# Kernel tuning notes

Hardware: AMD Instinct MI355X
Metric: run time of the kernel (lower is better)

The kernel has to match this reference:

```python
import jax, jax.numpy as jnp
import numpy as np

DIM = 512
MAX_STEP = 4
SLOTS = 8


def _lin(x, w, b):
    # torch nn.Linear convention: w is [out, in]
    return jnp.matmul(x, jnp.swapaxes(w, -1, -2)) + b


def setup_inputs() -> dict:
    B, L, HW, d, S, K = 512, 32, 196, DIM, MAX_STEP, SLOTS
    ks = iter(jax.random.split(jax.random.key(0), 48))
    def rn(shape, scale=1.0):
        return scale * jax.random.normal(next(ks), shape, dtype=jnp.float32)
    p = 0.05  # weight init scale
    z = lambda *s: jnp.zeros(s, jnp.float32)
    return {
        'context': rn((B, L, d)),
        'question': rn((B, 2 * d)),
        'knowledge': rn((B, d, HW)),
        'kb_proj': rn((B, d, HW)),
        'control': rn((B, d)),
        'memory': rn((B, d)),
        'history': rn((B, d, K)),
        'Wt_sequential': jnp.zeros((B, 1, K), jnp.float32).at[:, :, 0].set(1.0),
        # ControlUnit params (per-step position-aware linears, control-question linear, attention linear)
        'ctrl_pos_w': rn((S, d, 2 * d), p), 'ctrl_pos_b': z(S, d),
        'ctrl_cq_w': rn((d, 2 * d), p), 'ctrl_cq_b': z(d),
        'ctrl_attn_w': rn((1, d), p), 'ctrl_attn_b': z(1),
        # ReadUnit params (memory proj, concat proj, attention)
        'read_mem_w': rn((d, d), p), 'read_mem_b': z(d),
        'read_cat_w': rn((d, 2 * d), p), 'read_cat_b': z(d),
        'read_attn_w': rn((1, d), p), 'read_attn_b': z(1),
        # ReadMemory params (same structure, over the slot history)
        'rm_mem_w': rn((d, d), p), 'rm_mem_b': z(d),
        'rm_cat_w': rn((d, 2 * d), p), 'rm_cat_b': z(d),
        'rm_attn_w': rn((1, d), p), 'rm_attn_b': z(1),
        # WriteUnit (no self-attention / no memory gate)
        'write_w': rn((d, 2 * d), p), 'write_b': z(d),
        # linear_read gate MLP (2d -> 2d -> 1)
        'lr_w1': rn((2 * d, 2 * d), p), 'lr_b1': z(2 * d),
        'lr_w2': rn((1, 2 * d), p), 'lr_b2': z(1),
        # linear_read_history gate MLP
        'lrh_w1': rn((2 * d, 2 * d), p), 'lrh_b1': z(2 * d),
        'lrh_w2': rn((1, 2 * d), p), 'lrh_b2': z(1),
        # linear_layer_mix_context MLP (d -> d -> 3)
        'mix_w1': rn((d, d), p), 'mix_b1': z(d),
        'mix_w2': rn((3, d), p), 'mix_b2': z(3),
    }


def _forward(context, question, knowledge, kb_proj, control, memory, history, Wt_sequential,
             ctrl_pos_w, ctrl_pos_b, ctrl_cq_w, ctrl_cq_b, ctrl_attn_w, ctrl_attn_b,
             read_mem_w, read_mem_b, read_cat_w, read_cat_b, read_attn_w, read_attn_b,
             rm_mem_w, rm_mem_b, rm_cat_w, rm_cat_b, rm_attn_w, rm_attn_b,
             write_w, write_b, lr_w1, lr_b1, lr_w2, lr_b2,
             lrh_w1, lrh_b1, lrh_w2, lrh_b2, mix_w1, mix_b1, mix_w2, mix_b2):
    K = history.shape[2]
    # shift-by-one circulant matrix, matches the hard-coded convolution_kernel for slots in {4,6,8}
    conv_kernel = jnp.roll(jnp.eye(K, dtype=history.dtype), -1, axis=1)
    for i in range(MAX_STEP):
        # --- ControlUnit: attention over contextual words ---
        pa = _lin(question, ctrl_pos_w[i], ctrl_pos_b[i])                                  # [B,d]
        cqi = _lin(jnp.concatenate([control, pa], axis=1), ctrl_cq_w, ctrl_cq_b)           # [B,d]
        cvi = jax.nn.softmax(_lin(cqi[:, None, :] * context, ctrl_attn_w, ctrl_attn_b), axis=1)  # [B,L,1]
        control = jnp.sum(cvi * context, axis=1)                                           # [B,d]
        # --- ReadUnit: attention over the knowledge base ---
        mem_p = _lin(memory, read_mem_w, read_mem_b)[:, :, None]                           # [B,d,1]
        cat = jnp.concatenate([mem_p * kb_proj, kb_proj], axis=1)                          # [B,2d,HW]
        feat = _lin(cat.transpose(0, 2, 1), read_cat_w, read_cat_b)                        # [B,HW,d]
        attn = jax.nn.softmax(_lin(feat * control[:, None, :], read_attn_w, read_attn_b), axis=1)
        attn = attn.transpose(0, 2, 1)                                                     # [B,1,HW]
        read = jnp.sum(attn * knowledge, axis=2)                                           # [B,d]
        # --- ReadMemory: attention over the slot history ---
        memh = _lin(memory, rm_mem_w, rm_mem_b)[:, :, None]                                # [B,d,1]
        cath = jnp.concatenate([memh * history, history], axis=1)                          # [B,2d,K]
        feath = _lin(cath.transpose(0, 2, 1), rm_cat_w, rm_cat_b)                          # [B,K,d]
        rvi_h = jax.nn.softmax(_lin(feath * control[:, None, :], rm_attn_w, rm_attn_b), axis=1).transpose(0, 2, 1)  # [B,1,K]
        read_h = jnp.sum(rvi_h * history, axis=2)                                          # [B,d]
        # --- gates ---
        gkb = jax.nn.sigmoid(_lin(jax.nn.elu(_lin(jnp.concatenate([control, read], axis=1), lr_w1, lr_b1)), lr_w2, lr_b2))      # [B,1]
        gmem = jax.nn.sigmoid(_lin(jax.nn.elu(_lin(jnp.concatenate([control, read_h], axis=1), lrh_w1, lrh_b1)), lrh_w2, lrh_b2))  # [B,1]
        # --- gated addressable memory write (NTM-style) ---
        wts = Wt_sequential[:, 0, :]                                                       # [B,K]
        W = (gmem * rvi_h[:, 0, :] + wts * (1.0 - gmem)) * gkb                             # [B,K]
        history = history * (1.0 - W[:, None, :]) + read[:, :, None] * W[:, None, :]       # erase + add
        first = (1.0 - gmem) * gkb                                                         # [B,1]
        Wt_sequential = ((wts @ conv_kernel) * first + wts * (1.0 - first))[:, None, :]    # [B,1,K]
        # --- context mixing + write ---
        now_ctx = gkb * read
        last_ctx = gmem * read_h
        latest_ctx = (1.0 - gkb) * last_ctx + now_ctx
        cwv = jax.nn.softmax(_lin(jax.nn.elu(_lin(control, mix_w1, mix_b1)), mix_w2, mix_b2), axis=1)  # [B,3]
        ctx_read = cwv[:, 0:1] * now_ctx + cwv[:, 1:2] * last_ctx + cwv[:, 2:3] * latest_ctx
        memory = _lin(jnp.concatenate([ctx_read, memory], axis=1), write_w, write_b)       # [B,d]
    return memory


reference = _forward
```

## Files before the change

kernel.cpp:

```cpp
#include <hip/hip_runtime.h>
#include <cstddef>

constexpr int NB   = 512;
constexpr int ND   = 512;
constexpr int NL   = 32;
constexpr int NHW  = 196;
constexpr int NK   = 8;
constexpr int NSTEP = 4;

typedef __attribute__((ext_vector_type(8))) short short8v;
typedef __attribute__((ext_vector_type(4))) short short4v;
typedef __attribute__((ext_vector_type(4))) float f32x4;

__device__ __forceinline__ void splitbf(float x, short& h, short& l) {
    unsigned u  = __float_as_uint(x);
    unsigned hb = (u + 0x7FFFu + ((u >> 16) & 1u)) & 0xFFFF0000u;
    h = (short)(hb >> 16);
    float rem = x - __uint_as_float(hb);
    unsigned v = __float_as_uint(rem);
    l = (short)((v + 0x7FFFu + ((v >> 16) & 1u)) >> 16);
}

struct GP {
    const float* A1; const float* A2;
    const short* Bh; const short* Bl;
    const float* bias; float* C;
    int lda1, lda2, k1, N, K, ntN, tile0;
};
struct GP3 { GP p[3]; int np; };

template<int ACT>
__global__ __launch_bounds__(256) void ggemm_k(GP3 g)
{
    __shared__ short Ah[32][32], Al[32][32], Bh_s[64][32], Bl_s[64][32];
    const int flat = blockIdx.x;
    int pi = 0;
    if (g.np > 1 && flat >= g.p[1].tile0) pi = 1;
    if (g.np > 2 && flat >= g.p[2].tile0) pi = 2;
    const GP p = g.p[pi];
    const int local = flat - p.tile0;
    const int my = local / p.ntN;
    const int nx = local - my * p.ntN;
    const int m0 = my * 32, n0 = nx * 64;
    const int t = threadIdx.x, lane = t & 63, wid = t >> 6;
    const int wr = wid >> 1, wc = wid & 1;
    const int lr = lane & 15, lk = (lane >> 4) * 8;
    const int asr = t >> 3, asc = (t & 7) * 4;
    const int bsr = t >> 2, bsk = (t & 3) * 8;
    f32x4 acc0 = {}, acc1 = {};

    for (int kt = 0; kt < p.K; kt += 32) {
        {
            const int gk = kt + asc;
            const float* src = (gk < p.k1) ? p.A1 + (size_t)(m0 + asr) * p.lda1 + gk
                                           : p.A2 + (size_t)(m0 + asr) * p.lda2 + (gk - p.k1);
            float4 x = *(const float4*)src;
            short4v vh, vl; short hh, ll;
            splitbf(x.x, hh, ll); vh[0] = hh; vl[0] = ll;
            splitbf(x.y, hh, ll); vh[1] = hh; vl[1] = ll;
            splitbf(x.z, hh, ll); vh[2] = hh; vl[2] = ll;
            splitbf(x.w, hh, ll); vh[3] = hh; vl[3] = ll;
            *(short4v*)&Ah[asr][asc] = vh;
            *(short4v*)&Al[asr][asc] = vl;
        }
        {
            const size_t boff = (size_t)(n0 + bsr) * p.K + kt + bsk;
            *(short8v*)&Bh_s[bsr][bsk] = *(const short8v*)(p.Bh + boff);
            *(short8v*)&Bl_s[bsr][bsk] = *(const short8v*)(p.Bl + boff);
        }
        __syncthreads();
        short8v ah  = *(short8v*)&Ah[wr * 16 + lr][lk];
        short8v al  = *(short8v*)&Al[wr * 16 + lr][lk];
        short8v bh0 = *(short8v*)&Bh_s[wc * 32      + lr][lk];
        short8v bh1 = *(short8v*)&Bh_s[wc * 32 + 16 + lr][lk];
        short8v bl0 = *(short8v*)&Bl_s[wc * 32      + lr][lk];
        short8v bl1 = *(short8v*)&Bl_s[wc * 32 + 16 + lr][lk];
        acc0 = __builtin_amdgcn_mfma_f32_16x16x32_bf16(ah, bh0, acc0, 0, 0, 0);
        acc1 = __builtin_amdgcn_mfma_f32_16x16x32_bf16(ah, bh1, acc1, 0, 0, 0);
        acc0 = __builtin_amdgcn_mfma_f32_16x16x32_bf16(al, bh0, acc0, 0, 0, 0);
        acc1 = __builtin_amdgcn_mfma_f32_16x16x32_bf16(al, bh1, acc1, 0, 0, 0);
        acc0 = __builtin_amdgcn_mfma_f32_16x16x32_bf16(ah, bl0, acc0, 0, 0, 0);
        acc1 = __builtin_amdgcn_mfma_f32_16x16x32_bf16(ah, bl1, acc1, 0, 0, 0);
        __syncthreads();
    }
    const int r0 = m0 + wr * 16 + (lane >> 4) * 4;
    const int cb = n0 + wc * 32 + lr;
    #pragma unroll
    for (int fc = 0; fc < 2; ++fc) {
        const f32x4& a = fc ? acc1 : acc0;
        const int col = cb + fc * 16;
        float badd = p.bias ? p.bias[col] : 0.f;
        #pragma unroll
        for (int rr = 0; rr < 4; ++rr) {
            float x = a[rr] + badd;
            if (ACT == 1) x = (x > 0.f) ? x : (expf(x) - 1.f);
            p.C[(size_t)(r0 + rr) * p.N + col] = x;
        }
    }
}

struct WSeg { const float* src; short* dh; short* dl; int n; };
struct WTab { WSeg s[8]; int total; };

__global__ __launch_bounds__(256) void wconv_k(WTab tab)
{
    int i = blockIdx.x * 256 + threadIdx.x;
    if (i >= tab.total) return;
    int seg = 0, off = i;
    while (off >= tab.s[seg].n) { off -= tab.s[seg].n; ++seg; }
    short h, l; splitbf(tab.s[seg].src[off], h, l);
    tab.s[seg].dh[off] = h;
    tab.s[seg].dl[off] = l;
}

__global__ __launch_bounds__(256) void tconv_k(
    const float* s0, short* dh0, short* dl0,
    const float* s1, short* dh1, short* dl1)
{
    const float* src = blockIdx.z ? s1 : s0;
    short* dh = blockIdx.z ? dh1 : dh0;
    short* dl = blockIdx.z ? dl1 : dl0;
    __shared__ float tile[32][33];
    const int n0 = blockIdx.x * 32, k0 = blockIdx.y * 32;
    const int tx = threadIdx.x & 31, ty = threadIdx.x >> 5;
    for (int i = ty; i < 32; i += 8)
        tile[i][tx] = src[(size_t)(k0 + i) * 1024 + n0 + tx];
    __syncthreads();
    for (int i = ty; i < 32; i += 8) {
        short h, l; splitbf(tile[tx][i], h, l);
        dh[(size_t)(n0 + i) * 512 + k0 + tx] = h;
        dl[(size_t)(n0 + i) * 512 + k0 + tx] = l;
    }
}

__global__ __launch_bounds__(512) void ctrl_attn_k(
    const float* __restrict__ cqi, const float* __restrict__ context,
    const float* __restrict__ attn_w, const float* __restrict__ read_attn_w,
    const float* __restrict__ rm_attn_w,
    float* __restrict__ control, float* __restrict__ cw, float* __restrict__ cwh)
{
    const int b = blockIdx.x, t = threadIdx.x;
    const int lane = t & 63, w = t >> 6;
    __shared__ float q[ND];
    __shared__ float p[NL];
    const float* ctx = context + (size_t)b * NL * ND;

    q[t] = cqi[(size_t)b * ND + t] * attn_w[t];
    __syncthreads();

    for (int l = w; l < NL; l += 8) {
        float s = 0.f;
        const float* row = ctx + (size_t)l * ND;
        #pragma unroll
        for (int d = lane; d < ND; d += 64) s += q[d] * row[d];
        #pragma unroll
        for (int o = 32; o; o >>= 1) s += __shfl_down(s, o);
        if (lane == 0) p[l] = s;
    }
    __syncthreads();
    if (t == 0) {
        float mx = p[0];
        for (int l = 1; l < NL; ++l) mx = fmaxf(mx, p[l]);
        float sum = 0.f;
        for (int l = 0; l < NL; ++l) { float e = expf(p[l] - mx); p[l] = e; sum += e; }
        const float inv = 1.f / sum;
        for (int l = 0; l < NL; ++l) p[l] *= inv;
    }
    __syncthreads();
    float a = 0.f;
    #pragma unroll 8
    for (int l = 0; l < NL; ++l) a += p[l] * ctx[(size_t)l * ND + t];
    control[(size_t)b * ND + t] = a;
    cw [(size_t)b * ND + t] = a * read_attn_w[t];
    cwh[(size_t)b * ND + t] = a * rm_attn_w[t];
}

__global__ __launch_bounds__(256) void kbsh_k(
    const float* __restrict__ kb_proj, const float* __restrict__ mpc,
    const float* __restrict__ u, float* __restrict__ s_part,
    const float* __restrict__ hist, const float* __restrict__ uh,
    float* __restrict__ rvi, float* __restrict__ read_h)
{
    __shared__ float sh[NK * ND + ND];
    __shared__ float sred[NK], pk[NK];
    const int bx = blockIdx.x, t = threadIdx.x;
    const int lane = t & 63, w = t >> 6;

    if (bx < 4 * NB) {
        const int jc = bx >> 9, b = bx & 511;
        float* v = sh;
        const int j0 = jc * 128;
        if (t < 128) {
            const int j = j0 + t;
            v[t] = mpc[(size_t)b * 1024 + j] * u[(size_t)b * 1024 + j]
                 + u[(size_t)b * 1024 + 512 + j];
        }
        __syncthreads();
        if (t < NHW) {
            const float* base = kb_proj + (size_t)b * ND * NHW + (size_t)j0 * NHW + t;
            float s = 0.f;
            #pragma unroll 8
            for (int j = 0; j < 128; ++j) s += base[(size_t)j * NHW] * v[j];
            s_part[((size_t)jc * NB + b) * 200 + t] = s;
        }
    } else {
        const int b = bx - 4 * NB;
        float* ht = sh;
        float* vh = sh + NK * ND;
        const float* hb = hist + (size_t)b * ND * NK;

        for (int dd = t; dd < ND; dd += 256) {
            float4 h0 = *(const float4*)&hb[(size_t)dd * NK];
            float4 h1 = *(const float4*)&hb[(size_t)dd * NK + 4];
            ht[0 * ND + dd] = h0.x; ht[1 * ND + dd] = h0.y;
            ht[2 * ND + dd] = h0.z; ht[3 * ND + dd] = h0.w;
            ht[4 * ND + dd] = h1.x; ht[5 * ND + dd] = h1.y;
            ht[6 * ND + dd] = h1.z; ht[7 * ND + dd] = h1.w;
            vh[dd] = mpc[(size_t)b * 1024 + 512 + dd] * uh[(size_t)b * 1024 + dd]
                   + uh[(size_t)b * 1024 + 512 + dd];
        }
        __syncthreads();

        for (int k = w; k < NK; k += 4) {
            float s = 0.f;
            #pragma unroll 4
            for (int dd = lane; dd < ND; dd += 64) s += ht[k * ND + dd] * vh[dd];
            #pragma unroll
            for (int o = 32; o; o >>= 1) s += __shfl_down(s, o);
            if (lane == 0) sred[k] = s;
        }
        __syncthreads();
        if (t == 0) {
            float mx = sred[0];
            #pragma unroll
            for (int k = 1; k < NK; ++k) mx = fmaxf(mx, sred[k]);
            float ev[NK]; float sum = 0.f;
            #pragma unroll
            for (int k = 0; k < NK; ++k) { ev[k] = expf(sred[k] - mx); sum += ev[k]; }
            const float inv = 1.f / sum;
            #pragma unroll
            for (int k = 0; k < NK; ++k) { float pv = ev[k] * inv; pk[k] = pv; rvi[(size_t)b * NK + k] = pv; }
        }
        __syncthreads();
        for (int dd = t; dd < ND; dd += 256) {
            float a = 0.f;
            #pragma unroll
            for (int k = 0; k < NK; ++k) a += pk[k] * ht[k * ND + dd];
            read_h[(size_t)b * ND + dd] = a;
        }
    }
}

__global__ __launch_bounds__(256) void kb_read_k(
    const float* __restrict__ knowledge, const float* __restrict__ s_part,
    float* __restrict__ readv)
{
    const int dcb = blockIdx.x, b = blockIdx.y, t = threadIdx.x;
    const int lane = t & 63, w = t >> 6;
    __shared__ float ps[200];
    __shared__ float red[8];

    float val = -INFINITY;
    if (t < NHW) {
        float sp = 0.f;
        #pragma unroll
        for (int jc = 0; jc < 4; ++jc) sp += s_part[((size_t)jc * NB + b) * 200 + t];
        val = sp;
    }
    float mx = val;
    #pragma unroll
    for (int o = 32; o; o >>= 1) mx = fmaxf(mx, __shfl_xor(mx, o));
    if (lane == 0) red[w] = mx;
    __syncthreads();
    mx = fmaxf(fmaxf(red[0], red[1]), fmaxf(red[2], red[3]));
    const float e = (t < NHW) ? expf(val - mx) : 0.f;
    float sm = e;
    #pragma unroll
    for (int o = 32; o; o >>= 1) sm += __shfl_xor(sm, o);
    if (lane == 0) red[4 + w] = sm;
    __syncthreads();
    const float tot = red[4] + red[5] + red[6] + red[7];
    if (t < 200) ps[t] = (t < NHW) ? e / tot : 0.f;
    __syncthreads();

    const float* knw = knowledge + (size_t)b * ND * NHW;
    const int d1 = dcb * 64 + 64;
    for (int d = dcb * 64 + w; d < d1; d += 4) {
        const float* row = knw + (size_t)d * NHW;
        float a = 0.f;
        for (int h = lane; h < NHW; h += 64) a += ps[h] * row[h];
        #pragma unroll
        for (int o = 32; o; o >>= 1) a += __shfl_down(a, o);
        if (lane == 0) readv[(size_t)b * ND + d] = a;
    }
}

__global__ __launch_bounds__(256) void update2_k(
    const float* __restrict__ g1a, const float* __restrict__ g1b,
    const float* __restrict__ m1,
    const float* __restrict__ lr_w2,  const float* __restrict__ lr_b2,
    const float* __restrict__ lrh_w2, const float* __restrict__ lrh_b2,
    const float* __restrict__ mix_w2, const float* __restrict__ mix_b2,
    const float* __restrict__ rvi, const float* __restrict__ readv,
    const float* __restrict__ read_h,
    float* __restrict__ hist, float* __restrict__ wts, float* __restrict__ ctx_read)
{
    const int b = blockIdx.x, t = threadIdx.x;
    const int lane = t & 63, w = t >> 6;
    __shared__ float red[4][5];
    __shared__ float sc[5];

    float pa = 0.f, pb = 0.f, p0 = 0.f, p1 = 0.f, p2 = 0.f;
    for (int k = t; k < 2 * ND; k += 256) {
        pa += g1a[(size_t)b * 2 * ND + k] * lr_w2[k];
        pb += g1b[(size_t)b * 2 * ND + k] * lrh_w2[k];
    }
    for (int d = t; d < ND; d += 256) {
        const float m = m1[(size_t)b * ND + d];
        p0 += m * mix_w2[d];
        p1 += m * mix_w2[ND + d];
        p2 += m * mix_w2[2 * ND + d];
    }
    #pragma unroll
    for (int o = 32; o; o >>= 1) {
        pa += __shfl_down(pa, o); pb += __shfl_down(pb, o);
        p0 += __shfl_down(p0, o); p1 += __shfl_down(p1, o); p2 += __shfl_down(p2, o);
    }
    if (lane == 0) { red[w][0] = pa; red[w][1] = pb; red[w][2] = p0; red[w][3] = p1; red[w][4] = p2; }
    __syncthreads();
    if (t == 0) {
        float sa = 0.f, sb = 0.f, s0 = 0.f, s1 = 0.f, s2 = 0.f;
        #pragma unroll
        for (int i = 0; i < 4; ++i) { sa += red[i][0]; sb += red[i][1]; s0 += red[i][2]; s1 += red[i][3]; s2 += red[i][4]; }
        sc[0] = 1.f / (1.f + expf(-(sa + lr_b2[0])));
        sc[1] = 1.f / (1.f + expf(-(sb + lrh_b2[0])));
        const float l0 = s0 + mix_b2[0], l1 = s1 + mix_b2[1], l2 = s2 + mix_b2[2];
        const float mx = fmaxf(l0, fmaxf(l1, l2));
        const float e0 = expf(l0 - mx), e1 = expf(l1 - mx), e2 = expf(l2 - mx);
        const float inv = 1.f / (e0 + e1 + e2);
        sc[2] = e0 * inv; sc[3] = e1 * inv; sc[4] = e2 * inv;
    }
    __syncthreads();

    const float gk = sc[0], gm = sc[1];
    const float c0 = sc[2], c1 = sc[3], c2 = sc[4];
    __shared__ float wo[NK], Ws[NK];
    if (t < NK) {
        const float w_old = wts[(size_t)b * NK + t];
        wo[t] = w_old;
        Ws[t] = (gm * rvi[(size_t)b * NK + t] + w_old * (1.f - gm)) * gk;
    }
    __syncthreads();
    float Wr[NK];
    #pragma unroll
    for (int k = 0; k < NK; ++k) Wr[k] = Ws[k];

    for (int dd = t; dd < ND; dd += 256) {
        const float rd = readv[(size_t)b * ND + dd];
        const float rh = read_h[(size_t)b * ND + dd];
        const float now = gk * rd, last = gm * rh;
        const float latest = (1.f - gk) * last + now;
        ctx_read[(size_t)b * ND + dd] = c0 * now + c1 * last + c2 * latest;
        float* hp = hist + (size_t)b * ND * NK + (size_t)dd * NK;
        float4 h0 = *(const float4*)&hp[0];
        float4 h1 = *(const float4*)&hp[4];
        h0.x = h0.x * (1.f - Wr[0]) + rd * Wr[0];
        h0.y = h0.y * (1.f - Wr[1]) + rd * Wr[1];
        h0.z = h0.z * (1.f - Wr[2]) + rd * Wr[2];
        h0.w = h0.w * (1.f - Wr[3]) + rd * Wr[3];
        h1.x = h1.x * (1.f - Wr[4]) + rd * Wr[4];
        h1.y = h1.y * (1.f - Wr[5]) + rd * Wr[5];
        h1.z = h1.z * (1.f - Wr[6]) + rd * Wr[6];
        h1.w = h1.w * (1.f - Wr[7]) + rd * Wr[7];
        *(float4*)&hp[0] = h0;
        *(float4*)&hp[4] = h1;
    }
    if (t == 0) {
        const float first = (1.f - gm) * gk;
        float nw[NK];
        #pragma unroll
        for (int k = 0; k < NK; ++k) nw[k] = wo[(k + 1) & 7] * first + wo[k] * (1.f - first);
        #pragma unroll
        for (int k = 0; k < NK; ++k) wts[(size_t)b * NK + k] = nw[k];
    }
}

extern "C" void kernel_launch(void* const* d_in, const int* in_sizes, int n_in,
                              void* d_out, int out_size, void* d_ws, size_t ws_size,
                              hipStream_t stream)
{
    (void)in_sizes; (void)n_in; (void)out_size; (void)ws_size;
    const float* context    = (const float*)d_in[0];
    const float* question   = (const float*)d_in[1];
    const float* knowledge  = (const float*)d_in[2];
    const float* kb_proj    = (const float*)d_in[3];
    const float* control0   = (const float*)d_in[4];
    const float* memory0    = (const float*)d_in[5];
    const float* history0   = (const float*)d_in[6];
    const float* wt0        = (const float*)d_in[7];
    const float* ctrl_pos_w = (const float*)d_in[8];
    const float* ctrl_pos_b = (const float*)d_in[9];
    const float* ctrl_cq_w  = (const float*)d_in[10];
    const float* ctrl_cq_b  = (const float*)d_in[11];
    const float* ctrl_attn_w= (const float*)d_in[12];
    const float* read_mem_w = (const float*)d_in[14];
    const float* read_mem_b = (const float*)d_in[15];
    const float* read_cat_w = (const float*)d_in[16];
    const float* read_attn_w= (const float*)d_in[18];
    const float* rm_mem_w   = (const float*)d_in[20];
    const float* rm_mem_b   = (const float*)d_in[21];
    const float* rm_cat_w   = (const float*)d_in[22];
    const float* rm_attn_w  = (const float*)d_in[24];
    const float* write_w    = (const float*)d_in[26];
    const float* write_b    = (const float*)d_in[27];
    const float* lr_w1      = (const float*)d_in[28];
    const float* lr_b1      = (const float*)d_in[29];
    const float* lr_w2      = (const float*)d_in[30];
    const float* lr_b2      = (const float*)d_in[31];
    const float* lrh_w1     = (const float*)d_in[32];
    const float* lrh_b1     = (const float*)d_in[33];
    const float* lrh_w2     = (const float*)d_in[34];
    const float* lrh_b2     = (const float*)d_in[35];
    const float* mix_w1     = (const float*)d_in[36];
    const float* mix_b1     = (const float*)d_in[37];
    const float* mix_w2     = (const float*)d_in[38];
    const float* mix_b2     = (const float*)d_in[39];

    float* f = (float*)d_ws;
    auto takef = [&](size_t n) { float* p = f; f += n; return p; };
    float* pa_all = takef((size_t)NB * 2048);
    float* cqi    = takef((size_t)NB * ND);
    float* control= takef((size_t)NB * ND);
    float* cw     = takef((size_t)NB * ND);
    float* cwh    = takef((size_t)NB * ND);
    float* mpc    = takef((size_t)NB * 1024);
    float* u      = takef((size_t)NB * 1024);
    float* uh     = takef((size_t)NB * 1024);
    float* readv  = takef((size_t)NB * ND);
    float* read_h = takef((size_t)NB * ND);
    float* rvi    = takef((size_t)NB * NK);
    float* g1a    = takef((size_t)NB * 1024);
    float* g1b    = takef((size_t)NB * 1024);
    float* m1buf  = takef((size_t)NB * ND);
    float* ctx    = takef((size_t)NB * ND);
    float* hist   = takef((size_t)NB * ND * NK);
    float* wts    = takef((size_t)NB * NK);
    float* memA   = takef((size_t)NB * ND);
    float* memB   = takef((size_t)NB * ND);
    float* s_part = takef((size_t)4 * NB * 200);
    float* bcat   = takef(1024);

    short* s = (short*)f;
    auto takes = [&](size_t n) { short* p = s; s += n; return p; };
    short* cpw_h = takes((size_t)2048 * 1024); short* cpw_l = takes((size_t)2048 * 1024);
    short* cqw_h = takes((size_t)512 * 1024);  short* cqw_l = takes((size_t)512 * 1024);
    short* wmc_h = takes((size_t)1024 * 512);  short* wmc_l = takes((size_t)1024 * 512);
    short* rcw_h = takes((size_t)1024 * 512);  short* rcw_l = takes((size_t)1024 * 512);
    short* rmw_h = takes((size_t)1024 * 512);  short* rmw_l = takes((size_t)1024 * 512);
    short* lrw_h = takes((size_t)1024 * 1024); short* lrw_l = takes((size_t)1024 * 1024);
    short* lhw_h = takes((size_t)1024 * 1024); short* lhw_l = takes((size_t)1024 * 1024);
    short* mxw_h = takes((size_t)512 * 512);   short* mxw_l = takes((size_t)512 * 512);
    short* ww_h  = takes((size_t)512 * 1024);  short* ww_l  = takes((size_t)512 * 1024);

    hipMemcpyAsync(hist, history0, sizeof(float) * NB * ND * NK, hipMemcpyDeviceToDevice, stream);
    hipMemcpyAsync(wts,  wt0,      sizeof(float) * NB * NK,      hipMemcpyDeviceToDevice, stream);
    hipMemcpyAsync(bcat,       read_mem_b, sizeof(float) * 512, hipMemcpyDeviceToDevice, stream);
    hipMemcpyAsync(bcat + 512, rm_mem_b,   sizeof(float) * 512, hipMemcpyDeviceToDevice, stream);

    WTab tab;
    tab.s[0] = {ctrl_pos_w, cpw_h, cpw_l, 2048 * 1024};
    tab.s[1] = {ctrl_cq_w,  cqw_h, cqw_l, 512 * 1024};
    tab.s[2] = {read_mem_w, wmc_h, wmc_l, 512 * 512};
    tab.s[3] = {rm_mem_w,   wmc_h + 512 * 512, wmc_l + 512 * 512, 512 * 512};
    tab.s[4] = {lr_w1,  lrw_h, lrw_l, 1024 * 1024};
    tab.s[5] = {lrh_w1, lhw_h, lhw_l, 1024 * 1024};
    tab.s[6] = {mix_w1, mxw_h, mxw_l, 512 * 512};
    tab.s[7] = {write_w, ww_h, ww_l, 512 * 1024};
    tab.total = 2048*1024 + 512*1024 + 512*512 + 512*512 + 1024*1024 + 1024*1024 + 512*512 + 512*1024;
    wconv_k<<<dim3((tab.total + 255) / 256), dim3(256), 0, stream>>>(tab);
    tconv_k<<<dim3(32, 16, 2), dim3(256), 0, stream>>>(read_cat_w, rcw_h, rcw_l,
                                                       rm_cat_w,  rmw_h, rmw_l);

    auto P = [](const float* A1, const float* A2, int lda1, int lda2, int k1,
                const short* Bh, const short* Bl, const float* bias, float* C,
                int N, int K, int tile0) {
        GP q; q.A1 = A1; q.A2 = A2; q.Bh = Bh; q.Bl = Bl; q.bias = bias; q.C = C;
        q.lda1 = lda1; q.lda2 = lda2; q.k1 = k1; q.N = N; q.K = K;
        q.ntN = N / 64; q.tile0 = tile0;
        return q;
    };
    auto tilesOf = [](int N) { return (N / 64) * (NB / 32); };
    auto GG = [&](GP3 g, int total, int act) {
        if (act) ggemm_k<1><<<dim3(total), dim3(256), 0, stream>>>(g);
        else     ggemm_k<0><<<dim3(total), dim3(256), 0, stream>>>(g);
    };

    {
        GP3 g; g.np = 1;
        g.p[0] = P(question, question, 1024, 1024, 1024, cpw_h, cpw_l, ctrl_pos_b, pa_all, 2048, 1024, 0);
        GG(g, tilesOf(2048), 0);
    }

    const float* mems[5] = {memory0, memA, memB, memA, (float*)d_out};
    const float* ctrl_cur = control0;

    for (int i = 0; i < NSTEP; ++i) {
        {
            GP3 g; int nt = 0, np = 0;
            if (i > 0) {
                g.p[np++] = P(ctx, mems[i - 1], ND, ND, ND, ww_h, ww_l, write_b,
                              (float*)mems[i], ND, 1024, nt);
                nt += tilesOf(ND);
            }
            g.p[np++] = P(ctrl_cur, pa_all + (size_t)i * ND, ND, 2048, ND,
                          cqw_h, cqw_l, ctrl_cq_b, cqi, ND, 1024, nt);
            nt += tilesOf(ND);
            g.np = np;
            GG(g, nt, 0);
        }
        ctrl_attn_k<<<dim3(NB), dim3(512), 0, stream>>>(cqi, context, ctrl_attn_w,
                                                        read_attn_w, rm_attn_w, control, cw, cwh);
        ctrl_cur = control;
        {
            GP3 g; g.np = 3;
            g.p[0] = P(mems[i], mems[i], ND, ND, ND, wmc_h, wmc_l, bcat, mpc, 1024, 512, 0);
            g.p[1] = P(cw,  cw,  ND, ND, ND, rcw_h, rcw_l, nullptr, u,  1024, 512, 256);
            g.p[2] = P(cwh, cwh, ND, ND, ND, rmw_h, rmw_l, nullptr, uh, 1024, 512, 512);
            GG(g, 768, 0);
        }
        kbsh_k<<<dim3(5 * NB), dim3(256), 0, stream>>>(kb_proj, mpc, u, s_part,
                                                       hist, uh, rvi, read_h);
        kb_read_k<<<dim3(8, NB), dim3(256), 0, stream>>>(knowledge, s_part, readv);
        {
            GP3 g; g.np = 3;
            g.p[0] = P(control, readv,  ND, ND, ND, lrw_h, lrw_l, lr_b1,  g1a, 1024, 1024, 0);
            g.p[1] = P(control, read_h, ND, ND, ND, lhw_h, lhw_l, lrh_b1, g1b, 1024, 1024, 256);
            g.p[2] = P(control, control, ND, ND, ND, mxw_h, mxw_l, mix_b1, m1buf, 512, 512, 512);
            GG(g, 640, 1);
        }
        update2_k<<<dim3(NB), dim3(256), 0, stream>>>(g1a, g1b, m1buf,
                                                      lr_w2, lr_b2, lrh_w2, lrh_b2,
                                                      mix_w2, mix_b2, rvi, readv, read_h,
                                                      hist, wts, ctx);
    }
    {
        GP3 g; g.np = 1;
        g.p[0] = P(ctx, mems[3], ND, ND, ND, ww_h, ww_l, write_b, (float*)mems[4], ND, 1024, 0);
        GG(g, tilesOf(ND), 0);
    }
}
```

Before: 960.7 us.

## Pre-split GEMM activations to bf16 hi/lo and cache bf16 knowledge tensors

Producer kernels now write activations straight into bf16 high/low pairs. The GEMM loads its MFMA operands directly from global memory without LDS staging, splitting or barriers. On the first step, kb_proj and knowledge are also converted to single bf16 and stored. Later steps read those bf16 copies, halving the traffic over the large knowledge tensors. This reduces precision for the knowledge reads and drops LDS reuse in the GEMM, and it needs a larger workspace.

After: 1.216 ms. 1.27x slower.

```diff
diff --git a/kernel.cpp b/kernel.cpp
--- a/kernel.cpp
+++ b/kernel.cpp
@@ -9,7 +9,6 @@
 constexpr int NSTEP = 4;
 
 typedef __attribute__((ext_vector_type(8))) short short8v;
-typedef __attribute__((ext_vector_type(4))) short short4v;
 typedef __attribute__((ext_vector_type(4))) float f32x4;
 
 __device__ __forceinline__ void splitbf(float x, short& h, short& l) {
@@ -20,87 +19,90 @@
     unsigned v = __float_as_uint(rem);
     l = (short)((v + 0x7FFFu + ((v >> 16) & 1u)) >> 16);
 }
+__device__ __forceinline__ unsigned short f2bf(float x) {
+    unsigned u = __float_as_uint(x);
+    return (unsigned short)((u + 0x7FFFu + ((u >> 16) & 1u)) >> 16);
+}
+__device__ __forceinline__ float bf2f(unsigned short h) {
+    return __uint_as_float(((unsigned)h) << 16);
+}
 
 struct GP {
-    const float* A1; const float* A2;
-    const short* Bh; const short* Bl;
-    const float* bias; float* C;
+    const short *A1h, *A1l, *A2h, *A2l;
+    const short *Bh, *Bl;
+    const float* bias;
+    float* C; short* Ch; short* Cl;
     int lda1, lda2, k1, N, K, ntN, tile0;
 };
-struct GP3 { GP p[3]; int np; };
+struct GPG { GP p[3]; int np; };
 
 template<int ACT>
-__global__ __launch_bounds__(256) void ggemm_k(GP3 g)
-{
-    __shared__ short Ah[32][32], Al[32][32], Bh_s[64][32], Bl_s[64][32];
+__global__ __launch_bounds__(256) void ggemm_k(GPG g)
+{
     const int flat = blockIdx.x;
     int pi = 0;
     if (g.np > 1 && flat >= g.p[1].tile0) pi = 1;
     if (g.np > 2 && flat >= g.p[2].tile0) pi = 2;
     const GP p = g.p[pi];
     const int local = flat - p.tile0;
-    const int my = local / p.ntN;
-    const int nx = local - my * p.ntN;
+    const int my = local / p.ntN, nx = local - my * p.ntN;
     const int m0 = my * 32, n0 = nx * 64;
-    const int t = threadIdx.x, lane = t & 63, wid = t >> 6;
+    const int lane = threadIdx.x & 63, wid = threadIdx.x >> 6;
     const int wr = wid >> 1, wc = wid & 1;
     const int lr = lane & 15, lk = (lane >> 4) * 8;
-    const int asr = t >> 3, asc = (t & 7) * 4;
-    const int bsr = t >> 2, bsk = (t & 3) * 8;
+
+    const int arow = m0 + wr * 16 + lr;
+    const int br0  = n0 + wc * 32 + lr;
+    const short* b0h = p.Bh + (size_t)br0 * p.K + lk;
+    const short* b0l = p.Bl + (size_t)br0 * p.K + lk;
+    const short* b1h = b0h + (size_t)16 * p.K;
+    const short* b1l = b0l + (size_t)16 * p.K;
+    const short* a1h = p.A1h + (size_t)arow * p.lda1 + lk;
+    const short* a1l = p.A1l + (size_t)arow * p.lda1 + lk;
+    const short* a2h = p.A2h + (size_t)arow * p.lda2 + lk;
+    const short* a2l = p.A2l + (size_t)arow * p.lda2 + lk;
+
     f32x4 acc0 = {}, acc1 = {};
-
     for (int kt = 0; kt < p.K; kt += 32) {
-        {
-            const int gk = kt + asc;
-            const float* src = (gk < p.k1) ? p.A1 + (size_t)(m0 + asr) * p.lda1 + gk
-                                           : p.A2 + (size_t)(m0 + asr) * p.lda2 + (gk - p.k1);
-            float4 x = *(const float4*)src;
-            short4v vh, vl; short hh, ll;
-            splitbf(x.x, hh, ll); vh[0] = hh; vl[0] = ll;
-            splitbf(x.y, hh, ll); vh[1] = hh; vl[1] = ll;
-            splitbf(x.z, hh, ll); vh[2] = hh; vl[2] = ll;
-            splitbf(x.w, hh, ll); vh[3] = hh; vl[3] = ll;
-            *(short4v*)&Ah[asr][asc] = vh;
-            *(short4v*)&Al[asr][asc] = vl;
-        }
-        {
-            const size_t boff = (size_t)(n0 + bsr) * p.K + kt + bsk;
-            *(short8v*)&Bh_s[bsr][bsk] = *(const short8v*)(p.Bh + boff);
-            *(short8v*)&Bl_s[bsr][bsk] = *(const short8v*)(p.Bl + boff);
-        }
-        __syncthreads();
-        short8v ah  = *(short8v*)&Ah[wr * 16 + lr][lk];
-        short8v al  = *(short8v*)&Al[wr * 16 + lr][lk];
-        short8v bh0 = *(short8v*)&Bh_s[wc * 32      + lr][lk];
-        short8v bh1 = *(short8v*)&Bh_s[wc * 32 + 16 + lr][lk];
-        short8v bl0 = *(short8v*)&Bl_s[wc * 32      + lr][lk];
-        short8v bl1 = *(short8v*)&Bl_s[wc * 32 + 16 + lr][lk];
-        acc0 = __builtin_amdgcn_mfma_f32_16x16x32_bf16(ah, bh0, acc0, 0, 0, 0);
-        acc1 = __builtin_amdgcn_mfma_f32_16x16x32_bf16(ah, bh1, acc1, 0, 0, 0);
-        acc0 = __builtin_amdgcn_mfma_f32_16x16x32_bf16(al, bh0, acc0, 0, 0, 0);
-        acc1 = __builtin_amdgcn_mfma_f32_16x16x32_bf16(al, bh1, acc1, 0, 0, 0);
-        acc0 = __builtin_amdgcn_mfma_f32_16x16x32_bf16(ah, bl0, acc0, 0, 0, 0);
-        acc1 = __builtin_amdgcn_mfma_f32_16x16x32_bf16(ah, bl1, acc1, 0, 0, 0);
-        __syncthreads();
-    }
-    const int r0 = m0 + wr * 16 + (lane >> 4) * 4;
+        short8v ah, al;
+        if (kt < p.k1) {
+            ah = *(const short8v*)(a1h + kt);
+            al = *(const short8v*)(a1l + kt);
+        } else {
+            ah = *(const short8v*)(a2h + (kt - p.k1));
+            al = *(const short8v*)(a2l + (kt - p.k1));
+        }
+        short8v v0h = *(const short8v*)(b0h + kt);
+        short8v v0l = *(const short8v*)(b0l + kt);
+        short8v v1h = *(const short8v*)(b1h + kt);
+        short8v v1l = *(const short8v*)(b1l + kt);
+        acc0 = __builtin_amdgcn_mfma_f32_16x16x32_bf16(ah, v0h, acc0, 0, 0, 0);
+        acc1 = __builtin_amdgcn_mfma_f32_16x16x32_bf16(ah, v1h, acc1, 0, 0, 0);
+        acc0 = __builtin_amdgcn_mfma_f32_16x16x32_bf16(al, v0h, acc0, 0, 0, 0);
+        acc1 = __builtin_amdgcn_mfma_f32_16x16x32_bf16(al, v1h, acc1, 0, 0, 0);
+        acc0 = __builtin_amdgcn_mfma_f32_16x16x32_bf16(ah, v0l, acc0, 0, 0, 0);
+        acc1 = __builtin_amdgcn_mfma_f32_16x16x32_bf16(ah, v1l, acc1, 0, 0, 0);
+    }
+    const int r0 = m0 + wr * 16 + ((lane >> 4) << 2);
     const int cb = n0 + wc * 32 + lr;
     #pragma unroll
     for (int fc = 0; fc < 2; ++fc) {
         const f32x4& a = fc ? acc1 : acc0;
         const int col = cb + fc * 16;
-        float badd = p.bias ? p.bias[col] : 0.f;
+        const float badd = p.bias ? p.bias[col] : 0.f;
         #pragma unroll
         for (int rr = 0; rr < 4; ++rr) {
             float x = a[rr] + badd;
             if (ACT == 1) x = (x > 0.f) ? x : (expf(x) - 1.f);
-            p.C[(size_t)(r0 + rr) * p.N + col] = x;
+            const size_t idx = (size_t)(r0 + rr) * p.N + col;
+            if (p.C) p.C[idx] = x;
+            if (p.Ch) { short h, l; splitbf(x, h, l); p.Ch[idx] = h; p.Cl[idx] = l; }
         }
     }
 }
 
 struct WSeg { const float* src; short* dh; short* dl; int n; };
-struct WTab { WSeg s[8]; int total; };
+struct WTab { WSeg s[12]; int total; };
 
 __global__ __launch_bounds__(256) void wconv_k(WTab tab)
 {
@@ -137,7 +139,9 @@
     const float* __restrict__ cqi, const float* __restrict__ context,
     const float* __restrict__ attn_w, const float* __restrict__ read_attn_w,
     const float* __restrict__ rm_attn_w,
-    float* __restrict__ control, float* __restrict__ cw, float* __restrict__ cwh)
+    short* __restrict__ ct_h, short* __restrict__ ct_l,
+    short* __restrict__ cw_h, short* __restrict__ cw_l,
+    short* __restrict__ cx_h, short* __restrict__ cx_l)
 {
     const int b = blockIdx.x, t = threadIdx.x;
     const int lane = t & 63, w = t >> 6;
@@ -170,16 +174,21 @@
     float a = 0.f;
     #pragma unroll 8
     for (int l = 0; l < NL; ++l) a += p[l] * ctx[(size_t)l * ND + t];
-    control[(size_t)b * ND + t] = a;
-    cw [(size_t)b * ND + t] = a * read_attn_w[t];
-    cwh[(size_t)b * ND + t] = a * rm_attn_w[t];
-}
-
+    const size_t ix = (size_t)b * ND + t;
+    short h, l2;
+    splitbf(a, h, l2);                     ct_h[ix] = h; ct_l[ix] = l2;
+    splitbf(a * read_attn_w[t], h, l2);    cw_h[ix] = h; cw_l[ix] = l2;
+    splitbf(a * rm_attn_w[t],  h, l2);     cx_h[ix] = h; cx_l[ix] = l2;
+}
+
+template<int FIRST>
 __global__ __launch_bounds__(256) void kbsh_k(
-    const float* __restrict__ kb_proj, const float* __restrict__ mpc,
-    const float* __restrict__ u, float* __restrict__ s_part,
+    const float* __restrict__ kbp_f32, unsigned short* __restrict__ kbp_bf,
+    const float* __restrict__ mpc, const float* __restrict__ u,
+    float* __restrict__ s_part,
     const float* __restrict__ hist, const float* __restrict__ uh,
-    float* __restrict__ rvi, float* __restrict__ read_h)
+    float* __restrict__ rvi, float* __restrict__ read_h,
+    short* __restrict__ rh_h, short* __restrict__ rh_l)
 {
     __shared__ float sh[NK * ND + ND];
     __shared__ float sred[NK], pk[NK];
@@ -197,10 +206,19 @@
         }
         __syncthreads();
         if (t < NHW) {
-            const float* base = kb_proj + (size_t)b * ND * NHW + (size_t)j0 * NHW + t;
+            const size_t base = (size_t)b * ND * NHW + (size_t)j0 * NHW + t;
             float s = 0.f;
-            #pragma unroll 8
-            for (int j = 0; j < 128; ++j) s += base[(size_t)j * NHW] * v[j];
+            #pragma unroll 4
+            for (int j = 0; j < 128; ++j) {
+                float x;
+                if (FIRST) {
+                    x = kbp_f32[base + (size_t)j * NHW];
+                    kbp_bf[base + (size_t)j * NHW] = f2bf(x);
+                } else {
+                    x = bf2f(kbp_bf[base + (size_t)j * NHW]);
+                }
+                s += x * v[j];
+            }
             s_part[((size_t)jc * NB + b) * 200 + t] = s;
         }
     } else {
@@ -246,14 +264,19 @@
             float a = 0.f;
             #pragma unroll
             for (int k = 0; k < NK; ++k) a += pk[k] * ht[k * ND + dd];
-            read_h[(size_t)b * ND + dd] = a;
-        }
-    }
-}
-
+            const size_t ix = (size_t)b * ND + dd;
+            read_h[ix] = a;
+            short h, l; splitbf(a, h, l);
+            rh_h[ix] = h; rh_l[ix] = l;
+        }
+    }
+}
+
+template<int FIRST>
 __global__ __launch_bounds__(256) void kb_read_k(
-    const float* __restrict__ knowledge, const float* __restrict__ s_part,
-    float* __restrict__ readv)
+    const float* __restrict__ knw_f32, unsigned short* __restrict__ knw_bf,
+    const float* __restrict__ s_part,
+    float* __restrict__ readv, short* __restrict__ rv_h, short* __restrict__ rv_l)
 {
     const int dcb = blockIdx.x, b = blockIdx.y, t = threadIdx.x;
     const int lane = t & 63, w = t >> 6;
@@ -283,15 +306,28 @@
     if (t < 200) ps[t] = (t < NHW) ? e / tot : 0.f;
     __syncthreads();
 
-    const float* knw = knowledge + (size_t)b * ND * NHW;
     const int d1 = dcb * 64 + 64;
     for (int d = dcb * 64 + w; d < d1; d += 4) {
-        const float* row = knw + (size_t)d * NHW;
+        const size_t rbase = (size_t)b * ND * NHW + (size_t)d * NHW;
         float a = 0.f;
-        for (int h = lane; h < NHW; h += 64) a += ps[h] * row[h];
+        for (int h = lane; h < NHW; h += 64) {
+            float x;
+            if (FIRST) {
+                x = knw_f32[rbase + h];
+                knw_bf[rbase + h] = f2bf(x);
+            } else {
+                x = bf2f(knw_bf[rbase + h]);
+            }
+            a += ps[h] * x;
+        }
         #pragma unroll
         for (int o = 32; o; o >>= 1) a += __shfl_down(a, o);
-        if (lane == 0) readv[(size_t)b * ND + d] = a;
+        if (lane == 0) {
+            const size_t ix = (size_t)b * ND + d;
+            readv[ix] = a;
+            short h2, l2; splitbf(a, h2, l2);
+            rv_h[ix] = h2; rv_l[ix] = l2;
+        }
     }
 }
 
@@ -303,7 +339,8 @@
     const float* __restrict__ mix_w2, const float* __restrict__ mix_b2,
     const float* __restrict__ rvi, const float* __restrict__ readv,
     const float* __restrict__ read_h,
-    float* __restrict__ hist, float* __restrict__ wts, float* __restrict__ ctx_read)
+    float* __restrict__ hist, float* __restrict__ wts,
+    short* __restrict__ ctx_h, short* __restrict__ ctx_l)
 {
     const int b = blockIdx.x, t = threadIdx.x;
     const int lane = t & 63, w = t >> 6;
@@ -360,7 +397,10 @@
         const float rh = read_h[(size_t)b * ND + dd];
         const float now = gk * rd, last = gm * rh;
         const float latest = (1.f - gk) * last + now;
-        ctx_read[(size_t)b * ND + dd] = c0 * now + c1 * last + c2 * latest;
+        const float cr = c0 * now + c1 * last + c2 * latest;
+        short h2, l2; splitbf(cr, h2, l2);
+        ctx_h[(size_t)b * ND + dd] = h2;
+        ctx_l[(size_t)b * ND + dd] = l2;
         float* hp = hist + (size_t)b * ND * NK + (size_t)dd * NK;
         float4 h0 = *(const float4*)&hp[0];
         float4 h1 = *(const float4*)&hp[4];
@@ -428,11 +468,7 @@
 
     float* f = (float*)d_ws;
     auto takef = [&](size_t n) { float* p = f; f += n; return p; };
-    float* pa_all = takef((size_t)NB * 2048);
     float* cqi    = takef((size_t)NB * ND);
-    float* control= takef((size_t)NB * ND);
-    float* cw     = takef((size_t)NB * ND);
-    float* cwh    = takef((size_t)NB * ND);
     float* mpc    = takef((size_t)NB * 1024);
     float* u      = takef((size_t)NB * 1024);
     float* uh     = takef((size_t)NB * 1024);
@@ -442,15 +478,13 @@
     float* g1a    = takef((size_t)NB * 1024);
     float* g1b    = takef((size_t)NB * 1024);
     float* m1buf  = takef((size_t)NB * ND);
-    float* ctx    = takef((size_t)NB * ND);
     float* hist   = takef((size_t)NB * ND * NK);
     float* wts    = takef((size_t)NB * NK);
-    float* memA   = takef((size_t)NB * ND);
-    float* memB   = takef((size_t)NB * ND);
     float* s_part = takef((size_t)4 * NB * 200);
     float* bcat   = takef(1024);
 
-    short* s = (short*)f;
+    uintptr_t fa = ((uintptr_t)f + 15) & ~(uintptr_t)15;
+    short* s = (short*)fa;
     auto takes = [&](size_t n) { short* p = s; s += n; return p; };
     short* cpw_h = takes((size_t)2048 * 1024); short* cpw_l = takes((size_t)2048 * 1024);
     short* cqw_h = takes((size_t)512 * 1024);  short* cqw_l = takes((size_t)512 * 1024);
@@ -461,6 +495,21 @@
     short* lhw_h = takes((size_t)1024 * 1024); short* lhw_l = takes((size_t)1024 * 1024);
     short* mxw_h = takes((size_t)512 * 512);   short* mxw_l = takes((size_t)512 * 512);
     short* ww_h  = takes((size_t)512 * 1024);  short* ww_l  = takes((size_t)512 * 1024);
+    short* q_h   = takes((size_t)512 * 1024);  short* q_l   = takes((size_t)512 * 1024);
+    short* c0_h  = takes((size_t)NB * ND);     short* c0_l  = takes((size_t)NB * ND);
+    short* m0_h  = takes((size_t)NB * ND);     short* m0_l  = takes((size_t)NB * ND);
+    short* pa_h  = takes((size_t)NB * 2048);   short* pa_l  = takes((size_t)NB * 2048);
+    short* ct_h  = takes((size_t)NB * ND);     short* ct_l  = takes((size_t)NB * ND);
+    short* cw_h  = takes((size_t)NB * ND);     short* cw_l  = takes((size_t)NB * ND);
+    short* cwh_h = takes((size_t)NB * ND);     short* cwh_l = takes((size_t)NB * ND);
+    short* rv_h  = takes((size_t)NB * ND);     short* rv_l  = takes((size_t)NB * ND);
+    short* rh_h  = takes((size_t)NB * ND);     short* rh_l  = takes((size_t)NB * ND);
+    short* cx_h  = takes((size_t)NB * ND);     short* cx_l  = takes((size_t)NB * ND);
+    short* mA_h  = takes((size_t)NB * ND);     short* mA_l  = takes((size_t)NB * ND);
+    short* mB_h  = takes((size_t)NB * ND);     short* mB_l  = takes((size_t)NB * ND);
+    short* mC_h  = takes((size_t)NB * ND);     short* mC_l  = takes((size_t)NB * ND);
+    unsigned short* kbp_bf = (unsigned short*)s;
+    unsigned short* knw_bf = kbp_bf + (size_t)NB * ND * NHW;
 
     hipMemcpyAsync(hist, history0, sizeof(float) * NB * ND * NK, hipMemcpyDeviceToDevice, stream);
     hipMemcpyAsync(wts,  wt0,      sizeof(float) * NB * NK,      hipMemcpyDeviceToDevice, stream);
@@ -468,84 +517,112 @@
     hipMemcpyAsync(bcat + 512, rm_mem_b,   sizeof(float) * 512, hipMemcpyDeviceToDevice, stream);
 
     WTab tab;
-    tab.s[0] = {ctrl_pos_w, cpw_h, cpw_l, 2048 * 1024};
-    tab.s[1] = {ctrl_cq_w,  cqw_h, cqw_l, 512 * 1024};
-    tab.s[2] = {read_mem_w, wmc_h, wmc_l, 512 * 512};
-    tab.s[3] = {rm_mem_w,   wmc_h + 512 * 512, wmc_l + 512 * 512, 512 * 512};
-    tab.s[4] = {lr_w1,  lrw_h, lrw_l, 1024 * 1024};
-    tab.s[5] = {lrh_w1, lhw_h, lhw_l, 1024 * 1024};
-    tab.s[6] = {mix_w1, mxw_h, mxw_l, 512 * 512};
-    tab.s[7] = {write_w, ww_h, ww_l, 512 * 1024};
-    tab.total = 2048*1024 + 512*1024 + 512*512 + 512*512 + 1024*1024 + 1024*1024 + 512*512 + 512*1024;
+    tab.s[0]  = {ctrl_pos_w, cpw_h, cpw_l, 2048 * 1024};
+    tab.s[1]  = {ctrl_cq_w,  cqw_h, cqw_l, 512 * 1024};
+    tab.s[2]  = {read_mem_w, wmc_h, wmc_l, 512 * 512};
+    tab.s[3]  = {rm_mem_w,   wmc_h + 512 * 512, wmc_l + 512 * 512, 512 * 512};
+    tab.s[4]  = {lr_w1,  lrw_h, lrw_l, 1024 * 1024};
+    tab.s[5]  = {lrh_w1, lhw_h, lhw_l, 1024 * 1024};
+    tab.s[6]  = {mix_w1, mxw_h, mxw_l, 512 * 512};
+    tab.s[7]  = {write_w, ww_h, ww_l, 512 * 1024};
+    tab.s[8]  = {question, q_h, q_l, 512 * 1024};
+    tab.s[9]  = {control0, c0_h, c0_l, 512 * 512};
+    tab.s[10] = {memory0,  m0_h, m0_l, 512 * 512};
+    tab.s[11] = {nullptr, nullptr, nullptr, 0};
+    tab.total = 2048*1024 + 512*1024 + 512*512 + 512*512 + 1024*1024 + 1024*1024
+              + 512*512 + 512*1024 + 512*1024 + 512*512 + 512*512;
     wconv_k<<<dim3((tab.total + 255) / 256), dim3(256), 0, stream>>>(tab);
     tconv_k<<<dim3(32, 16, 2), dim3(256), 0, stream>>>(read_cat_w, rcw_h, rcw_l,
                                                        rm_cat_w,  rmw_h, rmw_l);
 
-    auto P = [](const float* A1, const float* A2, int lda1, int lda2, int k1,
-                const short* Bh, const short* Bl, const float* bias, float* C,
-                int N, int K, int tile0) {
-        GP q; q.A1 = A1; q.A2 = A2; q.Bh = Bh; q.Bl = Bl; q.bias = bias; q.C = C;
+    auto P = [](const short* A1h, const short* A1l, int lda1, int k1,
+                const short* A2h, const short* A2l, int lda2,
+                const short* Bh, const short* Bl, const float* bias,
+                float* C, short* Ch, short* Cl, int N, int K, int tile0) {
+        GP q; q.A1h = A1h; q.A1l = A1l; q.A2h = A2h; q.A2l = A2l;
+        q.Bh = Bh; q.Bl = Bl; q.bias = bias; q.C = C; q.Ch = Ch; q.Cl = Cl;
         q.lda1 = lda1; q.lda2 = lda2; q.k1 = k1; q.N = N; q.K = K;
         q.ntN = N / 64; q.tile0 = tile0;
         return q;
     };
-    auto tilesOf = [](int N) { return (N / 64) * (NB / 32); };
-    auto GG = [&](GP3 g, int total, int act) {
+    auto tilesOf = [](int N) { return (NB / 32) * (N / 64); };
+    auto GG = [&](GPG g, int total, int act) {
         if (act) ggemm_k<1><<<dim3(total), dim3(256), 0, stream>>>(g);
         else     ggemm_k<0><<<dim3(total), dim3(256), 0, stream>>>(g);
     };
 
     {
-        GP3 g; g.np = 1;
-        g.p[0] = P(question, question, 1024, 1024, 1024, cpw_h, cpw_l, ctrl_pos_b, pa_all, 2048, 1024, 0);
+        GPG g; g.np = 1;
+        g.p[0] = P(q_h, q_l, 1024, 1024, q_h, q_l, 1024, cpw_h, cpw_l, ctrl_pos_b,
+                   nullptr, pa_h, pa_l, 2048, 1024, 0);
         GG(g, tilesOf(2048), 0);
     }
 
-    const float* mems[5] = {memory0, memA, memB, memA, (float*)d_out};
-    const float* ctrl_cur = control0;
+    const short* mems_h[4] = {m0_h, mA_h, mB_h, mC_h};
+    const short* mems_l[4] = {m0_l, mA_l, mB_l, mC_l};
+    const short* ctl_h = c0_h;
+    const short* ctl_l = c0_l;
 
     for (int i = 0; i < NSTEP; ++i) {
         {
-            GP3 g; int nt = 0, np = 0;
+            GPG g; int nt = 0, np = 0;
             if (i > 0) {
-                g.p[np++] = P(ctx, mems[i - 1], ND, ND, ND, ww_h, ww_l, write_b,
-                              (float*)mems[i], ND, 1024, nt);
+                g.p[np++] = P(cx_h, cx_l, ND, ND, mems_h[i - 1], mems_l[i - 1], ND,
+                              ww_h, ww_l, write_b, nullptr,
+                              (short*)mems_h[i], (short*)mems_l[i], ND, 1024, nt);
                 nt += tilesOf(ND);
             }
-            g.p[np++] = P(ctrl_cur, pa_all + (size_t)i * ND, ND, 2048, ND,
-                          cqw_h, cqw_l, ctrl_cq_b, cqi, ND, 1024, nt);
+            g.p[np++] = P(ctl_h, ctl_l, ND, ND, pa_h + (size_t)i * ND, pa_l + (size_t)i * ND, 2048,
+                          cqw_h, cqw_l, ctrl_cq_b, cqi, nullptr, nullptr, ND, 1024, nt);
             nt += tilesOf(ND);
             g.np = np;
             GG(g, nt, 0);
         }
         ctrl_attn_k<<<dim3(NB), dim3(512), 0, stream>>>(cqi, context, ctrl_attn_w,
-                                                        read_attn_w, rm_attn_w, control, cw, cwh);
-        ctrl_cur = control;
+                                                        read_attn_w, rm_attn_w,
+                                                        ct_h, ct_l, cw_h, cw_l, cwh_h, cwh_l);
+        ctl_h = ct_h; ctl_l = ct_l;
         {
-            GP3 g; g.np = 3;
-            g.p[0] = P(mems[i], mems[i], ND, ND, ND, wmc_h, wmc_l, bcat, mpc, 1024, 512, 0);
-            g.p[1] = P(cw,  cw,  ND, ND, ND, rcw_h, rcw_l, nullptr, u,  1024, 512, 256);
-            g.p[2] = P(cwh, cwh, ND, ND, ND, rmw_h, rmw_l, nullptr, uh, 1024, 512, 512);
+            GPG g; g.np = 3;
+            g.p[0] = P(mems_h[i], mems_l[i], ND, ND, mems_h[i], mems_l[i], ND,
+                       wmc_h, wmc_l, bcat, mpc, nullptr, nullptr, 1024, 512, 0);
+            g.p[1] = P(cw_h, cw_l, ND, ND, cw_h, cw_l, ND,
+                       rcw_h, rcw_l, nullptr, u, nullptr, nullptr, 1024, 512, 256);
+            g.p[2] = P(cwh_h, cwh_l, ND, ND, cwh_h, cwh_l, ND,
+                       rmw_h, rmw_l, nullptr, uh, nullptr, nullptr, 1024, 512, 512);
             GG(g, 768, 0);
         }
-        kbsh_k<<<dim3(5 * NB), dim3(256), 0, stream>>>(kb_proj, mpc, u, s_part,
-                                                       hist, uh, rvi, read_h);
-        kb_read_k<<<dim3(8, NB), dim3(256), 0, stream>>>(knowledge, s_part, readv);
+        if (i == 0)
+            kbsh_k<1><<<dim3(5 * NB), dim3(256), 0, stream>>>(kb_proj, kbp_bf, mpc, u, s_part,
+                                                              hist, uh, rvi, read_h, rh_h, rh_l);
+        else
+            kbsh_k<0><<<dim3(5 * NB), dim3(256), 0, stream>>>(kb_proj, kbp_bf, mpc, u, s_part,
+                                                              hist, uh, rvi, read_h, rh_h, rh_l);
+        if (i == 0)
+            kb_read_k<1><<<dim3(8, NB), dim3(256), 0, stream>>>(knowledge, knw_bf, s_part,
+                                                                readv, rv_h, rv_l);
+        else
+            kb_read_k<0><<<dim3(8, NB), dim3(256), 0, stream>>>(knowledge, knw_bf, s_part,
+                                                                readv, rv_h, rv_l);
         {
-            GP3 g; g.np = 3;
-            g.p[0] = P(control, readv,  ND, ND, ND, lrw_h, lrw_l, lr_b1,  g1a, 1024, 1024, 0);
-            g.p[1] = P(control, read_h, ND, ND, ND, lhw_h, lhw_l, lrh_b1, g1b, 1024, 1024, 256);
-            g.p[2] = P(control, control, ND, ND, ND, mxw_h, mxw_l, mix_b1, m1buf, 512, 512, 512);
+            GPG g; g.np = 3;
+            g.p[0] = P(ct_h, ct_l, ND, ND, rv_h, rv_l, ND,
+                       lrw_h, lrw_l, lr_b1, g1a, nullptr, nullptr, 1024, 1024, 0);
+            g.p[1] = P(ct_h, ct_l, ND, ND, rh_h, rh_l, ND,
+                       lhw_h, lhw_l, lrh_b1, g1b, nullptr, nullptr, 1024, 1024, 256);
+            g.p[2] = P(ct_h, ct_l, ND, ND, ct_h, ct_l, ND,
+                       mxw_h, mxw_l, mix_b1, m1buf, nullptr, nullptr, 512, 512, 512);
             GG(g, 640, 1);
         }
         update2_k<<<dim3(NB), dim3(256), 0, stream>>>(g1a, g1b, m1buf,
                                                       lr_w2, lr_b2, lrh_w2, lrh_b2,
                                                       mix_w2, mix_b2, rvi, readv, read_h,
-                                                      hist, wts, ctx);
+                                                      hist, wts, cx_h, cx_l);
     }
     {
-        GP3 g; g.np = 1;
-        g.p[0] = P(ctx, mems[3], ND, ND, ND, ww_h, ww_l, write_b, (float*)mems[4], ND, 1024, 0);
+        GPG g; g.np = 1;
+        g.p[0] = P(cx_h, cx_l, ND, ND, mems_h[3], mems_l[3], ND,
+                   ww_h, ww_l, write_b, (float*)d_out, nullptr, nullptr, ND, 1024, 0);
         GG(g, tilesOf(ND), 0);
     }
 }
```
